# Performance work log

Measured on AMD Instinct MI355X. Metric: run time of the kernel, lower is better.

The kernel has to match this reference:

```python
import jax, jax.numpy as jnp
from jax import lax
import numpy as np

# --- static config (from module defaults / chosen shapes) ---
B, C, Hc, Wc = 16, 65, 160, 160
CELL = 8
H, W = Hc * CELL, Wc * CELL
NUM_KP = 512                          # num_keypoints
NMS_R = 8                             # nms_radius -> 17x17 window
MARGIN = 16                           # border_margin
NEG_INF = jnp.float32(-1e30)


def setup_inputs() -> dict:
    key = jax.random.key(0)
    heatmap = jax.random.normal(key, (B, C, Hc, Wc), dtype=jnp.float32)
    return {"heatmap": heatmap}


def _decode(heatmap):
    # softmax over 65 bins, drop dustbin -> (B, 64, Hc, Wc)
    prob = jax.nn.softmax(heatmap, axis=1)[:, :CELL * CELL]
    # pixel-shuffle to full-res score map (B, H, W)
    sm = (prob.transpose(0, 2, 3, 1)                 # (B,Hc,Wc,64)
              .reshape(B, Hc, Wc, CELL, CELL)
              .transpose(0, 1, 3, 2, 4)              # (B,Hc,8,Wc,8)
              .reshape(B, H, W))
    # border masking (zero outside margin)
    border = jnp.zeros((H, W), jnp.float32).at[MARGIN:H - MARGIN, MARGIN:W - MARGIN].set(1.0)
    sm = sm * border
    # 3x3 avg pool, stride 1, pad 1 (count_include_pad=True -> divide by 9)
    sm = lax.reduce_window(sm, 0.0, lax.add, (1, 3, 3), (1, 1, 1),
                           [(0, 0), (1, 1), (1, 1)]) / 9.0
    # NMS on detached scores: 17x17 max pool, -inf padding
    sm_d = lax.stop_gradient(sm)
    k = 2 * NMS_R + 1
    local_max = lax.reduce_window(sm_d, NEG_INF, lax.max, (1, k, k), (1, 1, 1),
                                  [(0, 0), (NMS_R, NMS_R), (NMS_R, NMS_R)])
    nms_mask = sm_d == local_max
    # suppress border band r = max(nms_radius, border_margin)
    r = max(NMS_R, MARGIN)
    interior = jnp.zeros((H, W), bool).at[r:H - r, r:W - r].set(True)
    nms_mask = nms_mask & interior
    # fixed-size top-k over masked flattened map (non-maxima get -inf)
    masked = jnp.where(nms_mask, sm_d, NEG_INF).reshape(B, H * W)
    _, top_idx = lax.top_k(masked, NUM_KP)           # (B, K)
    scores = jnp.take_along_axis(sm.reshape(B, H * W), top_idx, axis=1)  # (B,K)
    y = (top_idx // W).astype(jnp.float32)
    x = (top_idx % W).astype(jnp.float32)
    kp = jnp.stack([x, y], axis=-1)                  # (B, K, 2) in (x, y) px
    kp_norm = kp / jnp.array([W - 1, H - 1], jnp.float32)
    return kp_norm, scores


def reference(heatmap):
    return _decode(heatmap)
```

## Files before the change

kernel.cpp:

```cpp
#include <hip/hip_runtime.h>
#include <float.h>
#include <math.h>

#define BATCH 16
#define CHANS 65
#define HC 160
#define WC 160
#define HH 1280
#define WW 1280
#define KP 512
#define CAP 8192

static __device__ __forceinline__ unsigned long long make_key(float f, unsigned idx) {
  unsigned u = __float_as_uint(f);
  u = (u & 0x80000000u) ? ~u : (u | 0x80000000u);
  return ((unsigned long long)(~u) << 32) | (unsigned long long)idx;
}
static __device__ __forceinline__ float key_score(unsigned long long key) {
  unsigned mk = ~(unsigned)(key >> 32);
  unsigned u = (mk & 0x80000000u) ? (mk & 0x7FFFFFFFu) : ~mk;
  return __uint_as_float(u);
}

__global__ __launch_bounds__(256) void k_softmax_shuffle(const float* __restrict__ hm,
                                                         float* __restrict__ sm) {
  int id = blockIdx.x * 256 + threadIdx.x;
  const int NC = HC * WC;
  int b = id / NC;
  int cell = id - b * NC;
  int hc = cell / WC;
  int wc = cell - hc * WC;
  float* orow = sm + (size_t)b * HH * WW + (size_t)(hc * 8) * WW + wc * 8;

  if (hc < 2 || hc >= HC - 2 || wc < 2 || wc >= WC - 2) {
    float4 z = make_float4(0.f, 0.f, 0.f, 0.f);
#pragma unroll
    for (int r = 0; r < 8; ++r) {
      *(float4*)(orow + (size_t)r * WW) = z;
      *(float4*)(orow + (size_t)r * WW + 4) = z;
    }
    return;
  }

  const float* ibase = hm + (size_t)b * CHANS * NC + cell;
  float v[CHANS];
  float m = -FLT_MAX;
#pragma unroll
  for (int c = 0; c < CHANS; ++c) {
    v[c] = ibase[(size_t)c * NC];
    m = fmaxf(m, v[c]);
  }
  float s = 0.f;
#pragma unroll
  for (int c = 0; c < CHANS; ++c) {
    float d = __fsub_rn(v[c], m);
    v[c] = (float)exp((double)d);
    s = __fadd_rn(s, v[c]);
  }
#pragma unroll
  for (int r = 0; r < 8; ++r) {
    float4 q0, q1;
    q0.x = __fdiv_rn(v[r*8+0], s); q0.y = __fdiv_rn(v[r*8+1], s);
    q0.z = __fdiv_rn(v[r*8+2], s); q0.w = __fdiv_rn(v[r*8+3], s);
    q1.x = __fdiv_rn(v[r*8+4], s); q1.y = __fdiv_rn(v[r*8+5], s);
    q1.z = __fdiv_rn(v[r*8+6], s); q1.w = __fdiv_rn(v[r*8+7], s);
    *(float4*)(orow + (size_t)r * WW)     = q0;
    *(float4*)(orow + (size_t)r * WW + 4) = q1;
  }
}

__global__ __launch_bounds__(256) void k_avg(const float* __restrict__ sm,
                                             float* __restrict__ avg) {
  int id = blockIdx.x * 256 + threadIdx.x;
  const int WQ = WW / 4;
  int b = id / (HH * WQ);
  int rp = id - b * (HH * WQ);
  int y = rp / WQ;
  int x0 = (rp - y * WQ) * 4;
  const float* base = sm + (size_t)b * HH * WW;
  float a0 = 0.f, a1 = 0.f, a2 = 0.f, a3 = 0.f;
#pragma unroll
  for (int dy = -1; dy <= 1; ++dy) {
    int yy = y + dy;
    if (yy < 0 || yy >= HH) continue;
    const float* row = base + (size_t)yy * WW;
    float  l  = (x0 > 0) ? row[x0 - 1] : 0.f;
    float4 c4 = *(const float4*)(row + x0);
    float  rr = (x0 + 4 < WW) ? row[x0 + 4] : 0.f;
    a0 = __fadd_rn(__fadd_rn(__fadd_rn(a0, l),    c4.x), c4.y);
    a1 = __fadd_rn(__fadd_rn(__fadd_rn(a1, c4.x), c4.y), c4.z);
    a2 = __fadd_rn(__fadd_rn(__fadd_rn(a2, c4.y), c4.z), c4.w);
    a3 = __fadd_rn(__fadd_rn(__fadd_rn(a3, c4.z), c4.w), rr);
  }
  float4 o;
  o.x = __fdiv_rn(a0, 9.0f); o.y = __fdiv_rn(a1, 9.0f);
  o.z = __fdiv_rn(a2, 9.0f); o.w = __fdiv_rn(a3, 9.0f);
  *(float4*)(avg + (size_t)b * HH * WW + (size_t)y * WW + x0) = o;
}

#define CHUNKS 156
__global__ __launch_bounds__(320) void k_vmax_nms(const float* __restrict__ avg,
                                                  int* __restrict__ cnt,
                                                  unsigned long long* __restrict__ cand) {
  __shared__ float lv[8 * WW];
  __shared__ int scan[320];
  __shared__ int sbase;
  int b = blockIdx.x / CHUNKS;
  int chunk = blockIdx.x % CHUNKS;
  int y0 = 16 + 8 * chunk;
  int tid = threadIdx.x;
  int x0 = tid * 4;
  const float* base = avg + (size_t)b * HH * WW;

  float4 w[24];
#pragma unroll
  for (int j = 0; j < 24; ++j)
    w[j] = *(const float4*)(base + (size_t)(y0 - 8 + j) * WW + x0);
#pragma unroll
  for (int rr = 0; rr < 8; ++rr) {
    float4 mm = w[rr];
#pragma unroll
    for (int j = 1; j < 17; ++j) {
      float4 t = w[rr + j];
      mm.x = fmaxf(mm.x, t.x); mm.y = fmaxf(mm.y, t.y);
      mm.z = fmaxf(mm.z, t.z); mm.w = fmaxf(mm.w, t.w);
    }
    *(float4*)(lv + rr * WW + x0) = mm;
  }
  __syncthreads();

  unsigned msk0 = 0, msk1 = 0, msk2 = 0, msk3 = 0;
  int cntl = 0;
#pragma unroll
  for (int k = 0; k < 4; ++k) {
    int x = tid + 320 * k;
    if (x >= 16 && x < 1264) {
      unsigned m = 0;
#pragma unroll
      for (int rr = 0; rr < 8; ++rr) {
        const float* lrow = lv + rr * WW;
        float wm = lrow[x - 8];
#pragma unroll
        for (int j = 1; j < 17; ++j) wm = fmaxf(wm, lrow[x - 8 + j]);
        float c = base[(size_t)(y0 + rr) * WW + x];
        if (c >= wm) { m |= (1u << rr); cntl++; }
      }
      if (k == 0) msk0 = m; else if (k == 1) msk1 = m;
      else if (k == 2) msk2 = m; else msk3 = m;
    }
  }

  scan[tid] = cntl;
  __syncthreads();
  for (int off = 1; off < 320; off <<= 1) {
    int v = scan[tid];
    if (tid >= off) v += scan[tid - off];
    __syncthreads();
    scan[tid] = v;
    __syncthreads();
  }
  if (tid == 0) {
    int total = scan[319];
    sbase = total ? atomicAdd(&cnt[b * 16], total) : 0;
  }
  __syncthreads();
  int pos = sbase + scan[tid] - cntl;
#pragma unroll
  for (int k = 0; k < 4; ++k) {
    int x = tid + 320 * k;
    unsigned m = (k == 0) ? msk0 : (k == 1) ? msk1 : (k == 2) ? msk2 : msk3;
    while (m) {
      int rr = __ffs(m) - 1;
      m &= m - 1u;
      float c = base[(size_t)(y0 + rr) * WW + x];
      if (pos < CAP) cand[(size_t)b * CAP + pos] = make_key(c, (unsigned)((y0 + rr) * WW + x));
      pos++;
    }
  }
}

#define CE_ASC(A, B) { unsigned long long _x = s[A], _y = s[B]; \
                       if (_x > _y) { s[A] = _y; s[B] = _x; } }

__global__ __launch_bounds__(256) void k_sort_chunks(const int* __restrict__ cnt,
                                                     const unsigned long long* __restrict__ cand,
                                                     unsigned long long* __restrict__ srt) {
  __shared__ unsigned long long s[1024];
  int b = blockIdx.x >> 3;
  int c = blockIdx.x & 7;
  int tid = threadIdx.x;
  int raw = cnt[b * 16];
  int count = raw > CAP ? CAP : raw;
  int base = c * 1024;
  for (int i = tid; i < 1024; i += 256)
    s[i] = (base + i < count) ? cand[(size_t)b * CAP + base + i] : ~0ULL;
  __syncthreads();
  for (int k = 2; k <= 1024; k <<= 1) {
    for (int j = k >> 1; j > 0; j >>= 1) {
      for (int i = tid; i < 1024; i += 256) {
        int ixj = i ^ j;
        if (ixj > i) {
          unsigned long long a = s[i], d = s[ixj];
          bool up = ((i & k) == 0);
          if ((a > d) == up) { s[i] = d; s[ixj] = a; }
        }
      }
      __syncthreads();
    }
  }
  for (int i = tid; i < 1024; i += 256)
    srt[(size_t)b * CAP + base + i] = s[i];
}

__global__ __launch_bounds__(1024) void k_merge_topk(const int* __restrict__ cnt,
                                                     const unsigned long long* __restrict__ srt,
                                                     float* __restrict__ out) {
  __shared__ unsigned long long s[CAP];
  __shared__ unsigned flagw[32];
  int b = blockIdx.x;
  int tid = threadIdx.x;
  int raw = cnt[b * 16];
  int count = raw > CAP ? CAP : raw;
  if (tid < 32) flagw[tid] = 0;

#pragma unroll
  for (int c = 0; c < 8; ++c) {
    unsigned long long v = srt[(size_t)b * CAP + c * 1024 + tid];
    if (c & 1) s[c * 1024 + (1023 - tid)] = v;
    else       s[c * 1024 + tid]          = v;
  }
  __syncthreads();

#pragma unroll
  for (int r = 0; r < 4; ++r) { int i = r * 2048 + tid; CE_ASC(i, i + 1024); }
  __syncthreads();
  for (int j = 512; j >= 1; j >>= 1) {
    for (int t = tid; t < 2048; t += 1024) {
      int r = t >> 9, u = t & 511;
      int i = r * 2048 + (u / j) * (2 * j) + (u % j);
      CE_ASC(i, i + j);
    }
    __syncthreads();
  }
  {
    unsigned long long v1 = s[2048 + 1023 - tid];
    unsigned long long v2 = s[6144 + 1023 - tid];
    s[1024 + tid] = v1;
    s[5120 + tid] = v2;
  }
  __syncthreads();
#pragma unroll
  for (int r = 0; r < 2; ++r) { int i = r * 4096 + tid; CE_ASC(i, i + 1024); }
  __syncthreads();
  for (int j = 512; j >= 1; j >>= 1) {
    int r = tid >> 9, u = tid & 511;
    int i = r * 4096 + (u / j) * (2 * j) + (u % j);
    CE_ASC(i, i + j);
    __syncthreads();
  }
  s[1024 + tid] = s[4096 + 1023 - tid];
  __syncthreads();
  CE_ASC(tid, tid + 1024);
  __syncthreads();
  for (int j = 512; j >= 1; j >>= 1) {
    if (tid < 512) {
      int i = (tid / j) * (2 * j) + (tid % j);
      CE_ASC(i, i + j);
    }
    __syncthreads();
  }

  int lim = count < 520 ? count : 520;
  if (tid + 1 < lim) {
    unsigned u0 = ~(unsigned)(s[tid] >> 32);
    unsigned u1 = ~(unsigned)(s[tid + 1] >> 32);
    unsigned i0 = (unsigned)(s[tid] & 0xFFFFFFFFu);
    unsigned i1 = (unsigned)(s[tid + 1] & 0xFFFFFFFFu);
    if (u0 - u1 <= 1u && i0 > i1) atomicOr(&flagw[tid >> 5], 1u << (tid & 31));
  }
  __syncthreads();
  if (tid == 0) {
    int resume = 0;
    for (int w = 0; w < 17; ++w) {
      unsigned f = flagw[w];
      while (f) {
        int p = w * 32 + (__ffs(f) - 1);
        f &= f - 1u;
        if (p < resume) continue;
        int i = p;
        while (i + 1 < lim) {
          unsigned u0 = ~(unsigned)(s[i] >> 32);
          unsigned u1 = ~(unsigned)(s[i + 1] >> 32);
          unsigned i0 = (unsigned)(s[i] & 0xFFFFFFFFu);
          unsigned i1 = (unsigned)(s[i + 1] & 0xFFFFFFFFu);
          if (u0 - u1 <= 1u && i0 > i1) {
            unsigned long long t = s[i]; s[i] = s[i + 1]; s[i + 1] = t;
            ++i;
          } else break;
        }
        resume = i + 1;
      }
    }
  }
  __syncthreads();

  if (tid < KP) {
    if (tid < count) {
      unsigned long long key = s[tid];
      unsigned idx = (unsigned)(key & 0xFFFFFFFFu);
      float score = key_score(key);
      float xf = (float)(idx % WW);
      float yf = (float)(idx / WW);
      out[((size_t)b * KP + tid) * 2 + 0] = __fdiv_rn(xf, 1279.0f);
      out[((size_t)b * KP + tid) * 2 + 1] = __fdiv_rn(yf, 1279.0f);
      out[(size_t)BATCH * KP * 2 + (size_t)b * KP + tid] = score;
    } else {
      out[((size_t)b * KP + tid) * 2 + 0] = 2.0f;
      out[((size_t)b * KP + tid) * 2 + 1] = 2.0f;
      out[(size_t)BATCH * KP * 2 + (size_t)b * KP + tid] = 0.0f;
    }
    if (tid == 0 && raw > CAP) {
      out[((size_t)b * KP) * 2 + 0] = 3.0f;
      out[((size_t)b * KP) * 2 + 1] = 3.0f;
    }
  }
}

extern "C" void kernel_launch(void* const* d_in, const int* in_sizes, int n_in,
                              void* d_out, int out_size, void* d_ws, size_t ws_size,
                              hipStream_t stream) {
  const float* hm = (const float*)d_in[0];
  float* out = (float*)d_out;
  char* ws = (char*)d_ws;

  int* cnt = (int*)ws;
  unsigned long long* cand = (unsigned long long*)(ws + 1024);
  unsigned long long* srt  = cand + (size_t)BATCH * CAP;
  float* sm  = (float*)((char*)srt + (size_t)BATCH * CAP * 8);
  float* avg = sm + (size_t)BATCH * HH * WW;

  hipMemsetAsync(cnt, 0, 1024, stream);

  k_softmax_shuffle<<<BATCH * HC * WC / 256, 256, 0, stream>>>(hm, sm);
  k_avg<<<BATCH * HH * (WW / 4) / 256, 256, 0, stream>>>(sm, avg);
  k_vmax_nms<<<BATCH * CHUNKS, 320, 0, stream>>>(avg, cnt, cand);
  k_sort_chunks<<<BATCH * 8, 256, 0, stream>>>(cnt, cand, srt);
  k_merge_topk<<<BATCH, 1024, 0, stream>>>(cnt, srt, out);
}
```

Baseline: 235.4 us.

## Fuse 3x3 average pooling into the vertical-max NMS kernel

Removes the separate avg-pool kernel and its full-size intermediate buffer. Each NMS workgroup now computes the 3x3 box average on the fly for the 24 rows it needs, using a rolling 3-row window in registers, and keeps the 8 center rows in shared memory for the comparison and candidate emission. The block grows to 512 threads and the workgroup index is swizzled across the grid, probably for cache or XCD locality. In exchange, the halo rows are averaged redundantly across neighbouring chunks, and doubling shared memory to about 80 KB may lower occupancy.

Measured after the change: 247.8 us. 1.05x slower.

```diff
diff --git a/kernel.cpp b/kernel.cpp
--- a/kernel.cpp
+++ b/kernel.cpp
@@ -69,71 +69,70 @@
   }
 }
 
-__global__ __launch_bounds__(256) void k_avg(const float* __restrict__ sm,
-                                             float* __restrict__ avg) {
-  int id = blockIdx.x * 256 + threadIdx.x;
-  const int WQ = WW / 4;
-  int b = id / (HH * WQ);
-  int rp = id - b * (HH * WQ);
-  int y = rp / WQ;
-  int x0 = (rp - y * WQ) * 4;
-  const float* base = sm + (size_t)b * HH * WW;
-  float a0 = 0.f, a1 = 0.f, a2 = 0.f, a3 = 0.f;
-#pragma unroll
-  for (int dy = -1; dy <= 1; ++dy) {
-    int yy = y + dy;
-    if (yy < 0 || yy >= HH) continue;
-    const float* row = base + (size_t)yy * WW;
-    float  l  = (x0 > 0) ? row[x0 - 1] : 0.f;
-    float4 c4 = *(const float4*)(row + x0);
-    float  rr = (x0 + 4 < WW) ? row[x0 + 4] : 0.f;
-    a0 = __fadd_rn(__fadd_rn(__fadd_rn(a0, l),    c4.x), c4.y);
-    a1 = __fadd_rn(__fadd_rn(__fadd_rn(a1, c4.x), c4.y), c4.z);
-    a2 = __fadd_rn(__fadd_rn(__fadd_rn(a2, c4.y), c4.z), c4.w);
-    a3 = __fadd_rn(__fadd_rn(__fadd_rn(a3, c4.z), c4.w), rr);
-  }
-  float4 o;
-  o.x = __fdiv_rn(a0, 9.0f); o.y = __fdiv_rn(a1, 9.0f);
-  o.z = __fdiv_rn(a2, 9.0f); o.w = __fdiv_rn(a3, 9.0f);
-  *(float4*)(avg + (size_t)b * HH * WW + (size_t)y * WW + x0) = o;
-}
-
 #define CHUNKS 156
-__global__ __launch_bounds__(320) void k_vmax_nms(const float* __restrict__ avg,
-                                                  int* __restrict__ cnt,
-                                                  unsigned long long* __restrict__ cand) {
+__global__ __launch_bounds__(512) void k_avg_vmax_nms(const float* __restrict__ sm,
+                                                      int* __restrict__ cnt,
+                                                      unsigned long long* __restrict__ cand) {
   __shared__ float lv[8 * WW];
-  __shared__ int scan[320];
+  __shared__ float la[8 * WW];
+  __shared__ int scan[512];
   __shared__ int sbase;
-  int b = blockIdx.x / CHUNKS;
-  int chunk = blockIdx.x % CHUNKS;
+  int wgid = (blockIdx.x & 7) * 312 + (blockIdx.x >> 3);
+  int b = wgid / CHUNKS;
+  int chunk = wgid % CHUNKS;
   int y0 = 16 + 8 * chunk;
   int tid = threadIdx.x;
-  int x0 = tid * 4;
-  const float* base = avg + (size_t)b * HH * WW;
-
-  float4 w[24];
-#pragma unroll
-  for (int j = 0; j < 24; ++j)
-    w[j] = *(const float4*)(base + (size_t)(y0 - 8 + j) * WW + x0);
-#pragma unroll
-  for (int rr = 0; rr < 8; ++rr) {
-    float4 mm = w[rr];
-#pragma unroll
-    for (int j = 1; j < 17; ++j) {
-      float4 t = w[rr + j];
-      mm.x = fmaxf(mm.x, t.x); mm.y = fmaxf(mm.y, t.y);
-      mm.z = fmaxf(mm.z, t.z); mm.w = fmaxf(mm.w, t.w);
-    }
-    *(float4*)(lv + rr * WW + x0) = mm;
-  }
-  __syncthreads();
-
-  unsigned msk0 = 0, msk1 = 0, msk2 = 0, msk3 = 0;
+  const float* base = sm + (size_t)b * HH * WW;
+
+  if (tid < 320) {
+    int x0 = tid * 4;
+    float lf[3], rt[3];
+    float4 c4[3];
+    float4 mm[8];
+#pragma unroll
+    for (int k2 = 0; k2 < 26; ++k2) {
+      const float* row = base + (size_t)(y0 - 9 + k2) * WW;
+      int slot = k2 % 3;
+      lf[slot] = (x0 > 0) ? row[x0 - 1] : 0.f;
+      c4[slot] = *(const float4*)(row + x0);
+      rt[slot] = (x0 + 4 < WW) ? row[x0 + 4] : 0.f;
+      if (k2 >= 2) {
+        int k = k2 - 10;
+        float a0 = 0.f, a1 = 0.f, a2 = 0.f, a3 = 0.f;
+#pragma unroll
+        for (int d = 0; d < 3; ++d) {
+          int sl = (k2 - 2 + d) % 3;
+          float l = lf[sl], r = rt[sl];
+          float4 c = c4[sl];
+          a0 = __fadd_rn(__fadd_rn(__fadd_rn(a0, l),   c.x), c.y);
+          a1 = __fadd_rn(__fadd_rn(__fadd_rn(a1, c.x), c.y), c.z);
+          a2 = __fadd_rn(__fadd_rn(__fadd_rn(a2, c.y), c.z), c.w);
+          a3 = __fadd_rn(__fadd_rn(__fadd_rn(a3, c.z), c.w), r);
+        }
+        float4 a4;
+        a4.x = __fdiv_rn(a0, 9.0f); a4.y = __fdiv_rn(a1, 9.0f);
+        a4.z = __fdiv_rn(a2, 9.0f); a4.w = __fdiv_rn(a3, 9.0f);
+        if (k >= 0 && k < 8) *(float4*)(la + k * WW + x0) = a4;
+#pragma unroll
+        for (int rr = 0; rr < 8; ++rr) {
+          if (k == rr - 8) mm[rr] = a4;
+          else if (k > rr - 8 && k <= rr + 8) {
+            mm[rr].x = fmaxf(mm[rr].x, a4.x); mm[rr].y = fmaxf(mm[rr].y, a4.y);
+            mm[rr].z = fmaxf(mm[rr].z, a4.z); mm[rr].w = fmaxf(mm[rr].w, a4.w);
+          }
+        }
+      }
+    }
+#pragma unroll
+    for (int rr = 0; rr < 8; ++rr) *(float4*)(lv + rr * WW + x0) = mm[rr];
+  }
+  __syncthreads();
+
+  unsigned msk0 = 0, msk1 = 0, msk2 = 0;
   int cntl = 0;
 #pragma unroll
-  for (int k = 0; k < 4; ++k) {
-    int x = tid + 320 * k;
+  for (int k = 0; k < 3; ++k) {
+    int x = tid + 512 * k;
     if (x >= 16 && x < 1264) {
       unsigned m = 0;
 #pragma unroll
@@ -142,17 +141,16 @@
         float wm = lrow[x - 8];
 #pragma unroll
         for (int j = 1; j < 17; ++j) wm = fmaxf(wm, lrow[x - 8 + j]);
-        float c = base[(size_t)(y0 + rr) * WW + x];
+        float c = la[rr * WW + x];
         if (c >= wm) { m |= (1u << rr); cntl++; }
       }
-      if (k == 0) msk0 = m; else if (k == 1) msk1 = m;
-      else if (k == 2) msk2 = m; else msk3 = m;
+      if (k == 0) msk0 = m; else if (k == 1) msk1 = m; else msk2 = m;
     }
   }
 
   scan[tid] = cntl;
   __syncthreads();
-  for (int off = 1; off < 320; off <<= 1) {
+  for (int off = 1; off < 512; off <<= 1) {
     int v = scan[tid];
     if (tid >= off) v += scan[tid - off];
     __syncthreads();
@@ -160,19 +158,19 @@
     __syncthreads();
   }
   if (tid == 0) {
-    int total = scan[319];
+    int total = scan[511];
     sbase = total ? atomicAdd(&cnt[b * 16], total) : 0;
   }
   __syncthreads();
   int pos = sbase + scan[tid] - cntl;
 #pragma unroll
-  for (int k = 0; k < 4; ++k) {
-    int x = tid + 320 * k;
-    unsigned m = (k == 0) ? msk0 : (k == 1) ? msk1 : (k == 2) ? msk2 : msk3;
+  for (int k = 0; k < 3; ++k) {
+    int x = tid + 512 * k;
+    unsigned m = (k == 0) ? msk0 : (k == 1) ? msk1 : msk2;
     while (m) {
       int rr = __ffs(m) - 1;
       m &= m - 1u;
-      float c = base[(size_t)(y0 + rr) * WW + x];
+      float c = la[rr * WW + x];
       if (pos < CAP) cand[(size_t)b * CAP + pos] = make_key(c, (unsigned)((y0 + rr) * WW + x));
       pos++;
     }
@@ -337,13 +335,11 @@
   unsigned long long* cand = (unsigned long long*)(ws + 1024);
   unsigned long long* srt  = cand + (size_t)BATCH * CAP;
   float* sm  = (float*)((char*)srt + (size_t)BATCH * CAP * 8);
-  float* avg = sm + (size_t)BATCH * HH * WW;
 
   hipMemsetAsync(cnt, 0, 1024, stream);
 
   k_softmax_shuffle<<<BATCH * HC * WC / 256, 256, 0, stream>>>(hm, sm);
-  k_avg<<<BATCH * HH * (WW / 4) / 256, 256, 0, stream>>>(sm, avg);
-  k_vmax_nms<<<BATCH * CHUNKS, 320, 0, stream>>>(avg, cnt, cand);
+  k_avg_vmax_nms<<<BATCH * CHUNKS, 512, 0, stream>>>(sm, cnt, cand);
   k_sort_chunks<<<BATCH * 8, 256, 0, stream>>>(cnt, cand, srt);
   k_merge_topk<<<BATCH, 1024, 0, stream>>>(cnt, srt, out);
 }
```
